# Optimization experiments

Hardware: AMD Instinct MI355X
Metric: run time of the kernel (lower is better)

## Reference

```python
import jax, jax.numpy as jnp
import numpy as np

N = 4_194_304          # number of rays
DAMPING = 0.5          # LM(0.5)
MAX_DELTA = 1000.0     # clamp on LM step
N_ITER = 30            # no_grad warmup iterations
XMIN, XMAX, TAU = -1.0, 1.0, 1.0


def _surface_F(pts, c):
    # implicit parabolic rod: F(p) = x - c*(y^2 + z^2); pts: [N,3]
    return pts[..., 0] - c * (pts[..., 1] ** 2 + pts[..., 2] ** 2)


def _lm_delta(P, V, t, c):
    # Levenberg-Marquardt step for f(t) = F(P + t*V):
    # delta = f * f' / (f'^2 + damping), clamped to [-max_delta, max_delta]
    pts = P + t[:, None] * V                     # [N,3]
    f = _surface_F(pts, c)                       # [N]
    # f'(t) = gradF(pts) . V, gradF = (1, -2c*y, -2c*z)
    fp = V[:, 0] - 2.0 * c * (pts[:, 1] * V[:, 1] + pts[:, 2] * V[:, 2])
    delta = f * fp / (fp * fp + DAMPING)
    return jnp.clip(delta, -MAX_DELTA, MAX_DELTA)


def setup_inputs() -> dict:
    key = jax.random.key(0)
    k1, k2 = jax.random.split(key, 2)
    P = jax.random.normal(k1, (N, 3), jnp.float32) * 2.0
    V = jax.random.normal(k2, (N, 3), jnp.float32)
    V = V / jnp.linalg.norm(V, axis=-1, keepdims=True)
    a, b = 0.3, -0.2
    Rz = jnp.array([[np.cos(a), -np.sin(a), 0.0],
                    [np.sin(a),  np.cos(a), 0.0],
                    [0.0,        0.0,       1.0]], jnp.float32)
    Ry = jnp.array([[np.cos(b), 0.0, np.sin(b)],
                    [0.0,       1.0, 0.0],
                    [-np.sin(b), 0.0, np.cos(b)]], jnp.float32)
    R = Rz @ Ry                                  # rigid rotation [3,3]
    T = jnp.array([0.1, -0.2, 0.05], jnp.float32)
    c = jnp.float32(0.05)
    loss_in = jnp.float32(0.0)
    return {"P": P, "V": V, "R": R, "T": T, "c": c, "loss_in": loss_in}


def reference(P, V, R, T, c, loss_in):
    n = P.shape[0]
    # transform.inverse_points / inverse_vectors: R^T (p - T), R^T v
    P_local = (P - T) @ R                        # [N,3]
    V_local = V @ R                              # [N,3]

    # 30 no-grad LM iterations (torch.no_grad -> stop_gradient on inputs)
    Pl = jax.lax.stop_gradient(P_local)
    Vl = jax.lax.stop_gradient(V_local)
    cs = jax.lax.stop_gradient(c)

    def body(i, t):
        return t - _lm_delta(Pl, Vl, t, cs)

    t0 = jax.lax.fori_loop(0, N_ITER, body, jnp.zeros((n,), jnp.float32))

    # final differentiable LM step
    t = t0 - _lm_delta(P_local, V_local, t0, c)

    points_local = P_local + t[:, None] * V_local
    scale = jnp.mean(jnp.abs(jnp.array([XMIN, XMAX, TAU], jnp.float32)))
    F = _surface_F(points_local, c) / scale
    loss = loss_in + jnp.sum(F ** 2) / n
    return loss
```

## Files before the change

### kernel.cpp

```cpp
#include <hip/hip_runtime.h>
#include <stdint.h>


#define LM_ITERS 31
constexpr float DAMPING = 0.5f;

typedef __attribute__((address_space(3))) uint32_t lds_u32_t;
typedef __attribute__((address_space(1))) const uint32_t glob_u32_t;

__global__ __launch_bounds__(256) void rod_kernel(
    const float* __restrict__ P, const float* __restrict__ V,
    const float* __restrict__ Rm, const float* __restrict__ Tv,
    const float* __restrict__ c_ptr, double* __restrict__ ws, int n)
{
    const float c  = c_ptr[0];
    const float r00 = Rm[0], r01 = Rm[1], r02 = Rm[2];
    const float r10 = Rm[3], r11 = Rm[4], r12 = Rm[5];
    const float r20 = Rm[6], r21 = Rm[7], r22 = Rm[8];
    const float t0 = Tv[0], t1 = Tv[1], t2 = Tv[2];

    __shared__ float4 sh[4][192];

    const int lane = threadIdx.x & 63;
    const int wave = threadIdx.x >> 6;
    const int wave_ray_base = blockIdx.x * 1024 + wave * 256;
    const int base_ray      = wave_ray_base + 4 * lane;

    float px[4], py[4], pz[4], wx[4], wy[4], wz[4];

    if (wave_ray_base + 256 <= n) {
        const size_t wq = (size_t)(wave_ray_base >> 2) * 3;
        const char* gP = (const char*)P + wq * 16;
        const char* gV = (const char*)V + wq * 16;

        #pragma unroll
        for (int j = 0; j < 3; ++j) {
            __builtin_amdgcn_global_load_lds(
                (glob_u32_t*)(gP + (size_t)(j * 64 + lane) * 16),
                (lds_u32_t*)&sh[wave][j * 64 + lane], 16, 0, 0);
        }
        asm volatile("s_waitcnt vmcnt(0)" ::: "memory");
        const float4 pa = sh[wave][lane * 3 + 0];
        const float4 pb = sh[wave][lane * 3 + 1];
        const float4 pc = sh[wave][lane * 3 + 2];
        asm volatile("s_waitcnt lgkmcnt(0)" ::: "memory");

        #pragma unroll
        for (int j = 0; j < 3; ++j) {
            __builtin_amdgcn_global_load_lds(
                (glob_u32_t*)(gV + (size_t)(j * 64 + lane) * 16),
                (lds_u32_t*)&sh[wave][j * 64 + lane], 16, 0, 0);
        }
        asm volatile("s_waitcnt vmcnt(0)" ::: "memory");
        const float4 va = sh[wave][lane * 3 + 0];
        const float4 vb = sh[wave][lane * 3 + 1];
        const float4 vc = sh[wave][lane * 3 + 2];
        asm volatile("s_waitcnt lgkmcnt(0)" ::: "memory");

        px[0] = pa.x; px[1] = pa.w; px[2] = pb.z; px[3] = pc.y;
        py[0] = pa.y; py[1] = pb.x; py[2] = pb.w; py[3] = pc.z;
        pz[0] = pa.z; pz[1] = pb.y; pz[2] = pc.x; pz[3] = pc.w;
        wx[0] = va.x; wx[1] = va.w; wx[2] = vb.z; wx[3] = vc.y;
        wy[0] = va.y; wy[1] = vb.x; wy[2] = vb.w; wy[3] = vc.z;
        wz[0] = va.z; wz[1] = vb.y; wz[2] = vc.x; wz[3] = vc.w;
    } else {
        #pragma unroll
        for (int r = 0; r < 4; ++r) {
            const int ray = base_ray + r;
            if (ray < n) {
                px[r] = P[3 * ray + 0]; py[r] = P[3 * ray + 1]; pz[r] = P[3 * ray + 2];
                wx[r] = V[3 * ray + 0]; wy[r] = V[3 * ray + 1]; wz[r] = V[3 * ray + 2];
            } else {
                px[r] = py[r] = pz[r] = 0.0f;
                wx[r] = wy[r] = wz[r] = 0.0f;
            }
        }
    }

    float nA[4], f[4], fp[4];
    #pragma unroll
    for (int r = 0; r < 4; ++r) {
        const float qx = px[r] - t0, qy = py[r] - t1, qz = pz[r] - t2;
        const float plx = qx * r00 + qy * r10 + qz * r20;
        const float ply = qx * r01 + qy * r11 + qz * r21;
        const float plz = qx * r02 + qy * r12 + qz * r22;
        const float vlx = wx[r] * r00 + wy[r] * r10 + wz[r] * r20;
        const float vly = wx[r] * r01 + wy[r] * r11 + wz[r] * r21;
        const float vlz = wx[r] * r02 + wy[r] * r12 + wz[r] * r22;
        nA[r] = c * (vly * vly + vlz * vlz);
        f[r]  = plx - c * (ply * ply + plz * plz);
        fp[r] = vlx - 2.0f * c * (ply * vly + plz * vlz);
    }

    #pragma unroll 1
    for (int it = 0; it < LM_ITERS; ++it) {
        #pragma unroll
        for (int r = 0; r < 4; ++r) {
            const float den = fmaf(fp[r], fp[r], DAMPING);
            const float rcp = __builtin_amdgcn_rcpf(den);
            const float d   = (f[r] * fp[r]) * rcp;
            const float tmp = fmaf(nA[r], d, fp[r]);
            f[r]  = fmaf(-d, tmp, f[r]);
            fp[r] = fmaf(nA[r], d, tmp);
        }
    }

    double acc = 0.0;
    #pragma unroll
    for (int r = 0; r < 4; ++r)
        if (base_ray + r < n) acc += (double)f[r] * (double)f[r];

    for (int off = 32; off > 0; off >>= 1)
        acc += __shfl_down(acc, off, 64);
    __shared__ double sacc[4];
    if (lane == 0) sacc[wave] = acc;
    __syncthreads();
    if (threadIdx.x == 0) {
        atomicAdd(ws, sacc[0] + sacc[1] + sacc[2] + sacc[3]);
    }
}

__global__ void rod_finalize(const double* __restrict__ ws,
                             const float* __restrict__ loss_in,
                             float* __restrict__ out, double inv_n)
{
    out[0] = (float)(ws[0] * inv_n + (double)loss_in[0]);
}

extern "C" void kernel_launch(void* const* d_in, const int* in_sizes, int n_in,
                              void* d_out, int out_size, void* d_ws, size_t ws_size,
                              hipStream_t stream) {
    const float* P       = (const float*)d_in[0];
    const float* V       = (const float*)d_in[1];
    const float* R       = (const float*)d_in[2];
    const float* T       = (const float*)d_in[3];
    const float* c       = (const float*)d_in[4];
    const float* loss_in = (const float*)d_in[5];

    const int n = in_sizes[0] / 3;

    hipMemsetAsync(d_ws, 0, sizeof(double), stream);

    const int threads = (n + 3) / 4;
    const int block   = 256;
    const int grid    = (threads + block - 1) / block;
    rod_kernel<<<grid, block, 0, stream>>>(P, V, R, T, c, (double*)d_ws, n);
    rod_finalize<<<1, 1, 0, stream>>>((const double*)d_ws, loss_in,
                                      (float*)d_out, 1.0 / (double)n);
}
```

Measured before the change: 164.3 us.

## Process eight strided rays per thread and drop LDS-staged loads

Each thread now handles eight rays spaced 64 apart instead of four contiguous rays. The LDS-staged global_load_lds transpose is replaced by direct 12-byte struct loads from global memory, and the grid is halved to match. The intent is more independent work per thread to hide latency in the iteration loop and to drop the LDS round trip and waitcnt stalls. The cost is higher register pressure, which may lower occupancy, and possibly less efficient unaligned 12-byte loads.

```diff
diff --git a/kernel.cpp b/kernel.cpp
--- a/kernel.cpp
+++ b/kernel.cpp
@@ -1,12 +1,10 @@
 #include <hip/hip_runtime.h>
-#include <stdint.h>
 
 
 #define LM_ITERS 31
 constexpr float DAMPING = 0.5f;
 
-typedef __attribute__((address_space(3))) uint32_t lds_u32_t;
-typedef __attribute__((address_space(1))) const uint32_t glob_u32_t;
+struct F3 { float x, y, z; };
 
 __global__ __launch_bounds__(256) void rod_kernel(
     const float* __restrict__ P, const float* __restrict__ V,
@@ -19,74 +17,52 @@
     const float r20 = Rm[6], r21 = Rm[7], r22 = Rm[8];
     const float t0 = Tv[0], t1 = Tv[1], t2 = Tv[2];
 
-    __shared__ float4 sh[4][192];
-
     const int lane = threadIdx.x & 63;
     const int wave = threadIdx.x >> 6;
-    const int wave_ray_base = blockIdx.x * 1024 + wave * 256;
-    const int base_ray      = wave_ray_base + 4 * lane;
+    const int wbase = (blockIdx.x * 4 + wave) * 512;
 
-    float px[4], py[4], pz[4], wx[4], wy[4], wz[4];
+    const F3* __restrict__ P3 = (const F3*)P;
+    const F3* __restrict__ V3 = (const F3*)V;
 
-    if (wave_ray_base + 256 <= n) {
-        const size_t wq = (size_t)(wave_ray_base >> 2) * 3;
-        const char* gP = (const char*)P + wq * 16;
-        const char* gV = (const char*)V + wq * 16;
+    float px[8], py[8], pz[8], qx[8], qy[8], qz[8];
 
+    if (wbase + 512 <= n) {
         #pragma unroll
-        for (int j = 0; j < 3; ++j) {
-            __builtin_amdgcn_global_load_lds(
-                (glob_u32_t*)(gP + (size_t)(j * 64 + lane) * 16),
-                (lds_u32_t*)&sh[wave][j * 64 + lane], 16, 0, 0);
+        for (int r = 0; r < 8; ++r) {
+            const int ray = wbase + 64 * r + lane;
+            const F3 p = P3[ray];
+            px[r] = p.x; py[r] = p.y; pz[r] = p.z;
         }
-        asm volatile("s_waitcnt vmcnt(0)" ::: "memory");
-        const float4 pa = sh[wave][lane * 3 + 0];
-        const float4 pb = sh[wave][lane * 3 + 1];
-        const float4 pc = sh[wave][lane * 3 + 2];
-        asm volatile("s_waitcnt lgkmcnt(0)" ::: "memory");
-
         #pragma unroll
-        for (int j = 0; j < 3; ++j) {
-            __builtin_amdgcn_global_load_lds(
-                (glob_u32_t*)(gV + (size_t)(j * 64 + lane) * 16),
-                (lds_u32_t*)&sh[wave][j * 64 + lane], 16, 0, 0);
+        for (int r = 0; r < 8; ++r) {
+            const int ray = wbase + 64 * r + lane;
+            const F3 v = V3[ray];
+            qx[r] = v.x; qy[r] = v.y; qz[r] = v.z;
         }
-        asm volatile("s_waitcnt vmcnt(0)" ::: "memory");
-        const float4 va = sh[wave][lane * 3 + 0];
-        const float4 vb = sh[wave][lane * 3 + 1];
-        const float4 vc = sh[wave][lane * 3 + 2];
-        asm volatile("s_waitcnt lgkmcnt(0)" ::: "memory");
-
-        px[0] = pa.x; px[1] = pa.w; px[2] = pb.z; px[3] = pc.y;
-        py[0] = pa.y; py[1] = pb.x; py[2] = pb.w; py[3] = pc.z;
-        pz[0] = pa.z; pz[1] = pb.y; pz[2] = pc.x; pz[3] = pc.w;
-        wx[0] = va.x; wx[1] = va.w; wx[2] = vb.z; wx[3] = vc.y;
-        wy[0] = va.y; wy[1] = vb.x; wy[2] = vb.w; wy[3] = vc.z;
-        wz[0] = va.z; wz[1] = vb.y; wz[2] = vc.x; wz[3] = vc.w;
     } else {
         #pragma unroll
-        for (int r = 0; r < 4; ++r) {
-            const int ray = base_ray + r;
+        for (int r = 0; r < 8; ++r) {
+            const int ray = wbase + 64 * r + lane;
             if (ray < n) {
                 px[r] = P[3 * ray + 0]; py[r] = P[3 * ray + 1]; pz[r] = P[3 * ray + 2];
-                wx[r] = V[3 * ray + 0]; wy[r] = V[3 * ray + 1]; wz[r] = V[3 * ray + 2];
+                qx[r] = V[3 * ray + 0]; qy[r] = V[3 * ray + 1]; qz[r] = V[3 * ray + 2];
             } else {
                 px[r] = py[r] = pz[r] = 0.0f;
-                wx[r] = wy[r] = wz[r] = 0.0f;
+                qx[r] = qy[r] = qz[r] = 0.0f;
             }
         }
     }
 
-    float nA[4], f[4], fp[4];
+    float nA[8], f[8], fp[8];
     #pragma unroll
-    for (int r = 0; r < 4; ++r) {
-        const float qx = px[r] - t0, qy = py[r] - t1, qz = pz[r] - t2;
-        const float plx = qx * r00 + qy * r10 + qz * r20;
-        const float ply = qx * r01 + qy * r11 + qz * r21;
-        const float plz = qx * r02 + qy * r12 + qz * r22;
-        const float vlx = wx[r] * r00 + wy[r] * r10 + wz[r] * r20;
-        const float vly = wx[r] * r01 + wy[r] * r11 + wz[r] * r21;
-        const float vlz = wx[r] * r02 + wy[r] * r12 + wz[r] * r22;
+    for (int r = 0; r < 8; ++r) {
+        const float ax = px[r] - t0, ay = py[r] - t1, az = pz[r] - t2;
+        const float plx = ax * r00 + ay * r10 + az * r20;
+        const float ply = ax * r01 + ay * r11 + az * r21;
+        const float plz = ax * r02 + ay * r12 + az * r22;
+        const float vlx = qx[r] * r00 + qy[r] * r10 + qz[r] * r20;
+        const float vly = qx[r] * r01 + qy[r] * r11 + qz[r] * r21;
+        const float vlz = qx[r] * r02 + qy[r] * r12 + qz[r] * r22;
         nA[r] = c * (vly * vly + vlz * vlz);
         f[r]  = plx - c * (ply * ply + plz * plz);
         fp[r] = vlx - 2.0f * c * (ply * vly + plz * vlz);
@@ -95,7 +71,7 @@
     #pragma unroll 1
     for (int it = 0; it < LM_ITERS; ++it) {
         #pragma unroll
-        for (int r = 0; r < 4; ++r) {
+        for (int r = 0; r < 8; ++r) {
             const float den = fmaf(fp[r], fp[r], DAMPING);
             const float rcp = __builtin_amdgcn_rcpf(den);
             const float d   = (f[r] * fp[r]) * rcp;
@@ -107,8 +83,8 @@
 
     double acc = 0.0;
     #pragma unroll
-    for (int r = 0; r < 4; ++r)
-        if (base_ray + r < n) acc += (double)f[r] * (double)f[r];
+    for (int r = 0; r < 8; ++r)
+        if (wbase + 64 * r + lane < n) acc += (double)f[r] * (double)f[r];
 
     for (int off = 32; off > 0; off >>= 1)
         acc += __shfl_down(acc, off, 64);
@@ -141,7 +117,7 @@
 
     hipMemsetAsync(d_ws, 0, sizeof(double), stream);
 
-    const int threads = (n + 3) / 4;
+    const int threads = (n + 7) / 8;
     const int block   = 256;
     const int grid    = (threads + block - 1) / block;
     rod_kernel<<<grid, block, 0, stream>>>(P, V, R, T, c, (double*)d_ws, n);
```

Result: faster. 137.6 us (-16.2%).
